# Performance work log

Hardware: AMD Instinct MI355X
Metric: run time of the kernel (lower is better)

Reference implementation:

```python
import jax, jax.numpy as jnp
import numpy as np


def setup_inputs() -> dict:
    key = jax.random.key(0)
    k1, k2, k3, k4 = jax.random.split(key, 4)
    N, E, DIN, DOUT = 16384, 8192, 128, 128
    x = jax.random.normal(k1, (N, DIN), dtype=jnp.float32)
    # sparse binary incidence matrix, avg node degree ~ E * 0.005 ~ 41
    H = (jax.random.uniform(k2, (N, E)) < 0.005).astype(jnp.float32)
    W = jax.random.normal(k3, (DOUT, DIN), dtype=jnp.float32) * (1.0 / np.sqrt(DIN))
    b = jax.random.normal(k4, (DOUT,), dtype=jnp.float32) * 0.01
    return {"x": x, "H": H, "W": W, "b": b}


def reference(x, H, W, b):
    # Degree vectors. Original builds dense diag matrices; off-diagonal zeros
    # raised to negative powers become inf and are zeroed by nan_to_num, so the
    # math reduces to elementwise inverse powers of the degree vectors with
    # non-finite entries mapped to 0.
    deg_node = jnp.sum(H, axis=1)                    # [N]
    deg_edge = jnp.sum(H, axis=0)                    # [E]
    dvih = jnp.where(deg_node > 0, deg_node ** -0.5, 0.0)   # D_v^{-1/2}
    dei = jnp.where(deg_edge > 0, 1.0 / deg_edge, 0.0)      # D_e^{-1}
    # D_v^{-1/2} H D_e^{-1} H^T D_v^{-1/2} x, as broadcasted row scalings
    y = dvih[:, None] * x                            # [N, DIN]
    y = H.T @ y                                      # [E, DIN]
    y = dei[:, None] * y                             # [E, DIN]
    y = H @ y                                        # [N, DIN]
    y = dvih[:, None] * y                            # [N, DIN]
    return y @ W.T + b                               # [N, DOUT]
```

## Files before the change

### kernel.cpp

```cpp
#include <hip/hip_runtime.h>
#include <hip/hip_bf16.h>

#define NN 16384
#define EE 8192
#define DD 128
#define CSR_STRIDE 128
#define CSC_STRIDE 192


__global__ __launch_bounds__(256) void k1_parse(
    const float* __restrict__ H,
    float* __restrict__ dvih,
    int* __restrict__ csr_cnt,
    int* __restrict__ csr_idx,
    int* __restrict__ edge_cnt,
    int* __restrict__ csc_idx)
{
    const int n = blockIdx.x;
    const int t = threadIdx.x;
    __shared__ int s_cnt;
    __shared__ int s_list[CSR_STRIDE];
    if (t == 0) s_cnt = 0;
    __syncthreads();

    const float4* row = (const float4*)(H + (size_t)n * EE);
#pragma unroll
    for (int j = 0; j < 8; ++j) {
        int idx = t + 256 * j;
        float4 v = row[idx];
        int base = idx * 4;
        if (v.x != 0.0f) { int p = atomicAdd(&s_cnt, 1); if (p < CSR_STRIDE) s_list[p] = base + 0; }
        if (v.y != 0.0f) { int p = atomicAdd(&s_cnt, 1); if (p < CSR_STRIDE) s_list[p] = base + 1; }
        if (v.z != 0.0f) { int p = atomicAdd(&s_cnt, 1); if (p < CSR_STRIDE) s_list[p] = base + 2; }
        if (v.w != 0.0f) { int p = atomicAdd(&s_cnt, 1); if (p < CSR_STRIDE) s_list[p] = base + 3; }
    }
    __syncthreads();

    int cnt = s_cnt; if (cnt > CSR_STRIDE) cnt = CSR_STRIDE;
    if (t < cnt) {
        int e = s_list[t];
        csr_idx[(size_t)n * CSR_STRIDE + t] = e;
        int pos = atomicAdd(&edge_cnt[e], 1);
        if (pos < CSC_STRIDE) csc_idx[(size_t)e * CSC_STRIDE + pos] = n;
    }
    if (t == 0) {
        csr_cnt[n] = cnt;
        dvih[n] = (cnt > 0) ? (1.0f / sqrtf((float)cnt)) : 0.0f;
    }
}

__global__ __launch_bounds__(128) void k2_edge_gather(
    const float* __restrict__ x,
    const float* __restrict__ dvih,
    const int* __restrict__ edge_cnt,
    const int* __restrict__ csc_idx,
    float* __restrict__ y2)
{
    const int e = blockIdx.x;
    const int t = threadIdx.x;
    __shared__ int   s_lst[CSC_STRIDE];
    __shared__ float s_dv[CSC_STRIDE];

    int cnt = edge_cnt[e];
    int ccnt = cnt > CSC_STRIDE ? CSC_STRIDE : cnt;
    for (int i = t; i < ccnt; i += 128) {
        int n = csc_idx[(size_t)e * CSC_STRIDE + i];
        s_lst[i] = n;
        s_dv[i]  = dvih[n];
    }
    __syncthreads();

    float s = 0.0f;
    int i = 0;
    for (; i + 4 <= ccnt; i += 4) {
        int n0 = s_lst[i], n1 = s_lst[i+1], n2 = s_lst[i+2], n3 = s_lst[i+3];
        float f0 = s_dv[i], f1 = s_dv[i+1], f2 = s_dv[i+2], f3 = s_dv[i+3];
        float a0 = x[(size_t)n0 * DD + t];
        float a1 = x[(size_t)n1 * DD + t];
        float a2 = x[(size_t)n2 * DD + t];
        float a3 = x[(size_t)n3 * DD + t];
        s += f0*a0 + f1*a1 + f2*a2 + f3*a3;
    }
    for (; i < ccnt; ++i) s += s_dv[i] * x[(size_t)s_lst[i] * DD + t];

    float dei = (cnt > 0) ? (1.0f / (float)cnt) : 0.0f;
    y2[(size_t)e * DD + t] = s * dei;
}

__global__ __launch_bounds__(256) void k2b_gemm(
    const float* __restrict__ y2,
    const float* __restrict__ W,
    float* __restrict__ y2w)
{
    __shared__ float sA[32 * 132];
    __shared__ float sW[64 * 132];
    const int t = threadIdx.x;
    const int m0 = blockIdx.x * 32;

#pragma unroll
    for (int r = 0; r < 16; ++r) {
        int i = t + 256 * r;
        int row = i >> 7, col = i & 127;
        sA[row * 132 + col] = y2[(size_t)(m0 + row) * DD + col];
    }

    const int jg = t & 15;
    const int mg = t >> 4;
    const int m2 = mg * 2;
    const int j4 = jg * 4;

    for (int h = 0; h < 2; ++h) {
        __syncthreads();
#pragma unroll
        for (int r = 0; r < 32; ++r) {
            int i = t + 256 * r;
            int row = i >> 7, col = i & 127;
            sW[row * 132 + col] = W[(size_t)(h * 64 + row) * DD + col];
        }
        __syncthreads();

        float acc0[4] = {0.f, 0.f, 0.f, 0.f};
        float acc1[4] = {0.f, 0.f, 0.f, 0.f};
#pragma unroll 4
        for (int k = 0; k < 128; k += 4) {
            float4 a0 = *(const float4*)&sA[m2 * 132 + k];
            float4 a1 = *(const float4*)&sA[(m2 + 1) * 132 + k];
#pragma unroll
            for (int jj = 0; jj < 4; ++jj) {
                float4 w = *(const float4*)&sW[(j4 + jj) * 132 + k];
                acc0[jj] += a0.x*w.x + a0.y*w.y + a0.z*w.z + a0.w*w.w;
                acc1[jj] += a1.x*w.x + a1.y*w.y + a1.z*w.z + a1.w*w.w;
            }
        }
#pragma unroll
        for (int jj = 0; jj < 4; ++jj) {
            y2w[(size_t)(m0 + m2)     * DD + h * 64 + j4 + jj] = acc0[jj];
            y2w[(size_t)(m0 + m2 + 1) * DD + h * 64 + j4 + jj] = acc1[jj];
        }
    }
}

__global__ __launch_bounds__(128) void k3_node_gather(
    const float* __restrict__ y2w,
    const float* __restrict__ dvih,
    const int* __restrict__ csr_cnt,
    const int* __restrict__ csr_idx,
    const float* __restrict__ b,
    float* __restrict__ out)
{
    const int n = blockIdx.x;
    const int t = threadIdx.x;
    __shared__ int s_lst[CSR_STRIDE];

    int cnt = csr_cnt[n];
    if (t < cnt) s_lst[t] = csr_idx[(size_t)n * CSR_STRIDE + t];
    __syncthreads();

    float s = 0.0f;
    int i = 0;
    for (; i + 4 <= cnt; i += 4) {
        int e0 = s_lst[i], e1 = s_lst[i+1], e2 = s_lst[i+2], e3 = s_lst[i+3];
        s += y2w[(size_t)e0 * DD + t] + y2w[(size_t)e1 * DD + t]
           + y2w[(size_t)e2 * DD + t] + y2w[(size_t)e3 * DD + t];
    }
    for (; i < cnt; ++i) s += y2w[(size_t)s_lst[i] * DD + t];

    out[(size_t)n * DD + t] = dvih[n] * s + b[t];
}

extern "C" void kernel_launch(void* const* d_in, const int* in_sizes, int n_in,
                              void* d_out, int out_size, void* d_ws, size_t ws_size,
                              hipStream_t stream) {
    const float* x = (const float*)d_in[0];
    const float* H = (const float*)d_in[1];
    const float* W = (const float*)d_in[2];
    const float* b = (const float*)d_in[3];
    float* out = (float*)d_out;

    char* ws = (char*)d_ws;
    float* dvih    = (float*)(ws + 0);
    int*   csr_cnt = (int*)  (ws + 65536);
    int*   edge_cnt= (int*)  (ws + 131072);
    int*   csr_idx = (int*)  (ws + 163840);
    int*   csc_idx = (int*)  (ws + 8552448);
    float* y2      = (float*)(ws + 14843904);
    float* y2w     = (float*)(ws + 19038208);

    hipMemsetAsync(edge_cnt, 0, EE * sizeof(int), stream);

    k1_parse<<<NN, 256, 0, stream>>>(H, dvih, csr_cnt, csr_idx, edge_cnt, csc_idx);
    k2_edge_gather<<<EE, 128, 0, stream>>>(x, dvih, edge_cnt, csc_idx, y2);
    k2b_gemm<<<EE / 32, 256, 0, stream>>>(y2, W, y2w);
    k3_node_gather<<<NN, 128, 0, stream>>>(y2w, dvih, csr_cnt, csr_idx, b, out);
}
```

Baseline: 757.5 us.

## Apply weight GEMM to x before aggregation and fold memset into GEMM

Moves the linear projection to the front by computing x·W^T first, so the two sparse gathers work on projected features. This is valid by associativity, since the row scalings and H products commute with right-multiplication by W^T. The edge_cnt zeroing moves from a separate memset into the GEMM kernel, and the gather loops are unrolled to 8 with a partial sum. The GEMM now runs over N=16384 rows instead of E=8192, roughly doubling its FLOPs, in exchange for one fewer launch.

```diff
diff --git a/kernel.cpp b/kernel.cpp
--- a/kernel.cpp
+++ b/kernel.cpp
@@ -7,6 +7,65 @@
 #define CSR_STRIDE 128
 #define CSC_STRIDE 192
 
+
+__global__ __launch_bounds__(256) void g_gemm(
+    const float* __restrict__ x,
+    const float* __restrict__ W,
+    float* __restrict__ xw,
+    int* __restrict__ edge_cnt)
+{
+    const int t = threadIdx.x;
+    {
+        int tid = blockIdx.x * 256 + t;
+        if (tid < EE) edge_cnt[tid] = 0;
+    }
+
+    __shared__ float sA[32 * 132];
+    __shared__ float sW[64 * 132];
+    const int m0 = blockIdx.x * 32;
+
+#pragma unroll
+    for (int r = 0; r < 16; ++r) {
+        int i = t + 256 * r;
+        int row = i >> 7, col = i & 127;
+        sA[row * 132 + col] = x[(size_t)(m0 + row) * DD + col];
+    }
+
+    const int jg = t & 15;
+    const int mg = t >> 4;
+    const int m2 = mg * 2;
+    const int j4 = jg * 4;
+
+    for (int h = 0; h < 2; ++h) {
+        __syncthreads();
+#pragma unroll
+        for (int r = 0; r < 32; ++r) {
+            int i = t + 256 * r;
+            int row = i >> 7, col = i & 127;
+            sW[row * 132 + col] = W[(size_t)(h * 64 + row) * DD + col];
+        }
+        __syncthreads();
+
+        float acc0[4] = {0.f, 0.f, 0.f, 0.f};
+        float acc1[4] = {0.f, 0.f, 0.f, 0.f};
+#pragma unroll 4
+        for (int k = 0; k < 128; k += 4) {
+            float4 a0 = *(const float4*)&sA[m2 * 132 + k];
+            float4 a1 = *(const float4*)&sA[(m2 + 1) * 132 + k];
+#pragma unroll
+            for (int jj = 0; jj < 4; ++jj) {
+                float4 w = *(const float4*)&sW[(j4 + jj) * 132 + k];
+                acc0[jj] += a0.x*w.x + a0.y*w.y + a0.z*w.z + a0.w*w.w;
+                acc1[jj] += a1.x*w.x + a1.y*w.y + a1.z*w.z + a1.w*w.w;
+            }
+        }
+#pragma unroll
+        for (int jj = 0; jj < 4; ++jj) {
+            xw[(size_t)(m0 + m2)     * DD + h * 64 + j4 + jj] = acc0[jj];
+            xw[(size_t)(m0 + m2 + 1) * DD + h * 64 + j4 + jj] = acc1[jj];
+        }
+    }
+}
 
 __global__ __launch_bounds__(256) void k1_parse(
     const float* __restrict__ H,
@@ -50,7 +109,7 @@
 }
 
 __global__ __launch_bounds__(128) void k2_edge_gather(
-    const float* __restrict__ x,
+    const float* __restrict__ xw,
     const float* __restrict__ dvih,
     const int* __restrict__ edge_cnt,
     const int* __restrict__ csc_idx,
@@ -72,76 +131,22 @@
 
     float s = 0.0f;
     int i = 0;
-    for (; i + 4 <= ccnt; i += 4) {
-        int n0 = s_lst[i], n1 = s_lst[i+1], n2 = s_lst[i+2], n3 = s_lst[i+3];
-        float f0 = s_dv[i], f1 = s_dv[i+1], f2 = s_dv[i+2], f3 = s_dv[i+3];
-        float a0 = x[(size_t)n0 * DD + t];
-        float a1 = x[(size_t)n1 * DD + t];
-        float a2 = x[(size_t)n2 * DD + t];
-        float a3 = x[(size_t)n3 * DD + t];
-        s += f0*a0 + f1*a1 + f2*a2 + f3*a3;
-    }
-    for (; i < ccnt; ++i) s += s_dv[i] * x[(size_t)s_lst[i] * DD + t];
+    for (; i + 8 <= ccnt; i += 8) {
+        float partial = 0.0f;
+#pragma unroll
+        for (int u = 0; u < 8; ++u) {
+            partial += s_dv[i + u] * xw[(size_t)s_lst[i + u] * DD + t];
+        }
+        s += partial;
+    }
+    for (; i < ccnt; ++i) s += s_dv[i] * xw[(size_t)s_lst[i] * DD + t];
 
     float dei = (cnt > 0) ? (1.0f / (float)cnt) : 0.0f;
     y2[(size_t)e * DD + t] = s * dei;
 }
 
-__global__ __launch_bounds__(256) void k2b_gemm(
+__global__ __launch_bounds__(128) void k3_node_gather(
     const float* __restrict__ y2,
-    const float* __restrict__ W,
-    float* __restrict__ y2w)
-{
-    __shared__ float sA[32 * 132];
-    __shared__ float sW[64 * 132];
-    const int t = threadIdx.x;
-    const int m0 = blockIdx.x * 32;
-
-#pragma unroll
-    for (int r = 0; r < 16; ++r) {
-        int i = t + 256 * r;
-        int row = i >> 7, col = i & 127;
-        sA[row * 132 + col] = y2[(size_t)(m0 + row) * DD + col];
-    }
-
-    const int jg = t & 15;
-    const int mg = t >> 4;
-    const int m2 = mg * 2;
-    const int j4 = jg * 4;
-
-    for (int h = 0; h < 2; ++h) {
-        __syncthreads();
-#pragma unroll
-        for (int r = 0; r < 32; ++r) {
-            int i = t + 256 * r;
-            int row = i >> 7, col = i & 127;
-            sW[row * 132 + col] = W[(size_t)(h * 64 + row) * DD + col];
-        }
-        __syncthreads();
-
-        float acc0[4] = {0.f, 0.f, 0.f, 0.f};
-        float acc1[4] = {0.f, 0.f, 0.f, 0.f};
-#pragma unroll 4
-        for (int k = 0; k < 128; k += 4) {
-            float4 a0 = *(const float4*)&sA[m2 * 132 + k];
-            float4 a1 = *(const float4*)&sA[(m2 + 1) * 132 + k];
-#pragma unroll
-            for (int jj = 0; jj < 4; ++jj) {
-                float4 w = *(const float4*)&sW[(j4 + jj) * 132 + k];
-                acc0[jj] += a0.x*w.x + a0.y*w.y + a0.z*w.z + a0.w*w.w;
-                acc1[jj] += a1.x*w.x + a1.y*w.y + a1.z*w.z + a1.w*w.w;
-            }
-        }
-#pragma unroll
-        for (int jj = 0; jj < 4; ++jj) {
-            y2w[(size_t)(m0 + m2)     * DD + h * 64 + j4 + jj] = acc0[jj];
-            y2w[(size_t)(m0 + m2 + 1) * DD + h * 64 + j4 + jj] = acc1[jj];
-        }
-    }
-}
-
-__global__ __launch_bounds__(128) void k3_node_gather(
-    const float* __restrict__ y2w,
     const float* __restrict__ dvih,
     const int* __restrict__ csr_cnt,
     const int* __restrict__ csr_idx,
@@ -158,12 +163,15 @@
 
     float s = 0.0f;
     int i = 0;
-    for (; i + 4 <= cnt; i += 4) {
-        int e0 = s_lst[i], e1 = s_lst[i+1], e2 = s_lst[i+2], e3 = s_lst[i+3];
-        s += y2w[(size_t)e0 * DD + t] + y2w[(size_t)e1 * DD + t]
-           + y2w[(size_t)e2 * DD + t] + y2w[(size_t)e3 * DD + t];
-    }
-    for (; i < cnt; ++i) s += y2w[(size_t)s_lst[i] * DD + t];
+    for (; i + 8 <= cnt; i += 8) {
+        float partial = 0.0f;
+#pragma unroll
+        for (int u = 0; u < 8; ++u) {
+            partial += y2[(size_t)s_lst[i + u] * DD + t];
+        }
+        s += partial;
+    }
+    for (; i < cnt; ++i) s += y2[(size_t)s_lst[i] * DD + t];
 
     out[(size_t)n * DD + t] = dvih[n] * s + b[t];
 }
@@ -183,13 +191,11 @@
     int*   edge_cnt= (int*)  (ws + 131072);
     int*   csr_idx = (int*)  (ws + 163840);
     int*   csc_idx = (int*)  (ws + 8552448);
-    float* y2      = (float*)(ws + 14843904);
-    float* y2w     = (float*)(ws + 19038208);
-
-    hipMemsetAsync(edge_cnt, 0, EE * sizeof(int), stream);
-
+    float* xw      = (float*)(ws + 14843904);
+    float* y2      = (float*)(ws + 23232512);
+
+    g_gemm<<<NN / 32, 256, 0, stream>>>(x, W, xw, edge_cnt);
     k1_parse<<<NN, 256, 0, stream>>>(H, dvih, csr_cnt, csr_idx, edge_cnt, csc_idx);
-    k2_edge_gather<<<EE, 128, 0, stream>>>(x, dvih, edge_cnt, csc_idx, y2);
-    k2b_gemm<<<EE / 32, 256, 0, stream>>>(y2, W, y2w);
-    k3_node_gather<<<NN, 128, 0, stream>>>(y2w, dvih, csr_cnt, csr_idx, b, out);
-}
+    k2_edge_gather<<<EE, 128, 0, stream>>>(xw, dvih, edge_cnt, csc_idx, y2);
+    k3_node_gather<<<NN, 128, 0, stream>>>(y2, dvih, csr_cnt, csr_idx, b, out);
+}
```

Result: no change. 767.4 us (+1.3%).
